# Kernel optimization log

Hardware: AMD Instinct MI355X
Metric: run time of the kernel (lower is better)

The kernel has to match this reference:

```python
import jax, jax.numpy as jnp
import numpy as np

NUM_HEADS = 8
POOL = 4  # kq_downscale kernel/stride (spatial)
B, S, H, W, C = 32, 8, 32, 32, 128
TOTAL_KEY_DEPTH = 512
VAL_FILTERS = 128
OUT_FILTERS = 64


def _avg_pool(x):
    # tf.nn.avg_pool3d with kernel/stride [1,1,4,4,1], SAME padding (dims divide evenly)
    win = (1, 1, POOL, POOL, 1)
    s = jax.lax.reduce_window(x, 0.0, jax.lax.add, win, win, 'SAME')
    return s / (POOL * POOL)


def _conv2d(x, w, b):
    # TimeDistributed Conv2D, same padding. x: (B,S,H,W,Cin), w: (kh,kw,Cin,Cout)
    Bx, Sx, Hx, Wx, Cx = x.shape
    y = jax.lax.conv_general_dilated(
        x.reshape(Bx * Sx, Hx, Wx, Cx), w, (1, 1), 'SAME',
        dimension_numbers=('NHWC', 'HWIO', 'NHWC'))
    return y.reshape(Bx, Sx, Hx, Wx, -1) + b


def _rel_emb(length_q, length_k, max_rel, table):
    # _generate_relative_positions_embeddings
    rk = jnp.arange(length_k)
    rq = rk[-length_q:]
    idx = jnp.clip(rk[None, :] - rq[:, None], -max_rel, max_rel) + max_rel
    return table[idx]  # (Lq, Lk, depth)


def setup_inputs() -> dict:
    key = jax.random.key(0)
    ks = jax.random.split(key, 11)
    qk_in = (H // POOL) * (W // POOL) * C          # 8*8*128 = 8192
    d_vh = H * W * VAL_FILTERS // NUM_HEADS         # 16384 per-head value depth
    d_kh = TOTAL_KEY_DEPTH // NUM_HEADS             # 64
    return {
        'inputs': jax.random.normal(ks[0], (B, 1, H, W, C), jnp.float32),
        'k_antecedent': jax.random.normal(ks[1], (B, S, H, W, C), jnp.float32),
        'v_antecedent': jax.random.normal(ks[2], (B, S, H, W, C), jnp.float32),
        'w_q': jax.random.normal(ks[3], (qk_in, TOTAL_KEY_DEPTH), jnp.float32) * 0.02,
        'w_k': jax.random.normal(ks[4], (qk_in, TOTAL_KEY_DEPTH), jnp.float32) * 0.02,
        'conv_v_w': jax.random.normal(ks[5], (3, 3, C, VAL_FILTERS), jnp.float32) * 0.02,
        'conv_v_b': jnp.zeros((VAL_FILTERS,), jnp.float32),
        'conv_o_w': jax.random.normal(ks[6], (3, 3, VAL_FILTERS, OUT_FILTERS), jnp.float32) * 0.02,
        'conv_o_b': jnp.zeros((OUT_FILTERS,), jnp.float32),
        'table_k': jax.random.normal(ks[7], (S, d_kh), jnp.float32) * 0.05,
        'table_v': jax.random.normal(ks[8], (S, d_vh), jnp.float32) * 0.05,
    }


def reference(inputs, k_antecedent, v_antecedent, w_q, w_k,
              conv_v_w, conv_v_b, conv_o_w, conv_o_b, table_k, table_v):
    Bx, Sx, Hx, Wx, Cx = v_antecedent.shape
    nh = NUM_HEADS
    max_rel = Sx // 2 - 1  # attn_factor_reduc/2 - 1

    # downscale + flatten q/k antecedents
    q_a = _avg_pool(inputs).reshape(Bx, 1, -1)
    k_a = _avg_pool(k_antecedent).reshape(Bx, Sx, -1)
    q = q_a @ w_q                   # (B,1,Dk)
    k = k_a @ w_k                   # (B,S,Dk)
    v = _conv2d(v_antecedent, conv_v_w, conv_v_b).reshape(Bx, Sx, -1)  # (B,S,Dv)

    def split(x):  # (B,L,D) -> (B,h,L,D/h)
        Bz, L, D = x.shape
        return x.reshape(Bz, L, nh, D // nh).transpose(0, 2, 1, 3)

    q, k, v = split(q), split(k), split(v)
    q = q * (q.shape[-1] ** -0.5)

    # relative-position logits: _relative_attention_inner(q, k, z_k, transpose=True)
    z_k = _rel_emb(1, Sx, max_rel, table_k)  # (1,S,dkh)
    logits = jnp.einsum('bhqd,bhkd->bhqk', q, k) + jnp.einsum('bhqd,qkd->bhqk', q, z_k)
    weights = jax.nn.softmax(logits, axis=-1)  # (B,h,1,S)

    # relative values: _relative_attention_inner(weights, v, z_v, transpose=False)
    z_v = _rel_emb(1, Sx, max_rel, table_v)  # (1,S,dvh)
    x = jnp.einsum('bhqk,bhkd->bhqd', weights, v) + jnp.einsum('bhqk,qkd->bhqd', weights, z_v)

    # combine heads, restore spatial shape, output conv
    x = x.transpose(0, 2, 1, 3).reshape(Bx, 1, Hx, Wx, -1)  # (B,1,H,W,Fv)
    out = _conv2d(x, conv_o_w, conv_o_b)                     # (B,1,H,W,Fo)
    return out
```

## Files before the change

### kernel.cpp

```cpp
#include <hip/hip_runtime.h>
#include <hip/hip_bf16.h>

typedef __hip_bfloat16 bf16;
typedef __attribute__((ext_vector_type(8))) short bf16x8;
typedef __attribute__((ext_vector_type(4))) float f32x4;

constexpr int B_ = 32, S_ = 8, H_ = 32, W_ = 32, C_ = 128;
constexpr int NH_ = 8, KD_ = 512, DKH_ = 64, VF_ = 128, OF_ = 64;
constexpr int QKIN_ = 8192;

static __device__ __forceinline__ short bfbits(float f) {
    bf16 h = __float2bfloat16(f);
    short s;
    __builtin_memcpy(&s, &h, 2);
    return s;
}
static __device__ __forceinline__ unsigned int packbf2(float a, float b) {
    return ((unsigned int)(unsigned short)bfbits(b) << 16) | (unsigned short)bfbits(a);
}

__global__ void k_zero(float* __restrict__ p, int n) {
    int i = blockIdx.x * 256 + threadIdx.x;
    if (i < n) p[i] = 0.f;
}

__global__ void k_pool4(const float* __restrict__ in, short* __restrict__ out, int n_img) {
    int idx = blockIdx.x * 256 + threadIdx.x;
    if (idx >= n_img * 2048) return;
    int c4 = (idx & 31) * 4;
    int pw = (idx >> 5) & 7;
    int ph = (idx >> 8) & 7;
    int img = idx >> 11;
    const float* p = in + (((size_t)img * H_ + ph * 4) * W_ + pw * 4) * C_ + c4;
    float4 s = {0.f, 0.f, 0.f, 0.f};
#pragma unroll
    for (int dy = 0; dy < 4; ++dy)
#pragma unroll
        for (int dx = 0; dx < 4; ++dx) {
            float4 v = *reinterpret_cast<const float4*>(p + (dy * W_ + dx) * C_);
            s.x += v.x; s.y += v.y; s.z += v.z; s.w += v.w;
        }
    uint2 pk;
    pk.x = packbf2(s.x * 0.0625f, s.y * 0.0625f);
    pk.y = packbf2(s.z * 0.0625f, s.w * 0.0625f);
    *reinterpret_cast<uint2*>(out + (size_t)img * QKIN_ + (ph * 8 + pw) * 128 + c4) = pk;
}

__global__ __launch_bounds__(256) void k_wT(const float* __restrict__ w,
                                            short* __restrict__ wT) {
    __shared__ float t[64][65];
    int k0 = blockIdx.x * 64, n0 = blockIdx.y * 64;
    int col = threadIdx.x & 63, r4 = threadIdx.x >> 6;
#pragma unroll
    for (int i = 0; i < 16; ++i) {
        int kr = i * 4 + r4;
        t[kr][col] = w[(size_t)(k0 + kr) * KD_ + n0 + col];
    }
    __syncthreads();
    int n = threadIdx.x >> 3, kg = threadIdx.x & 7;
#pragma unroll
    for (int half = 0; half < 2; ++half) {
        int nn = n + half * 32;
        short v[8];
#pragma unroll
        for (int j = 0; j < 8; ++j) v[j] = bfbits(t[kg * 8 + j][nn]);
        *reinterpret_cast<bf16x8*>(wT + (size_t)(n0 + nn) * QKIN_ + k0 + kg * 8) =
            *reinterpret_cast<bf16x8*>(v);
    }
}

__global__ __launch_bounds__(256) void k_gemm_mfma(const short* __restrict__ A,
                                                   const short* __restrict__ WT,
                                                   float* __restrict__ out) {
    int wave = threadIdx.x >> 6, lane = threadIdx.x & 63;
    int quad = lane >> 4, l15 = lane & 15;
    int m0 = blockIdx.x * 32;
    int n0 = blockIdx.y * 128 + wave * 32;
    int k0 = blockIdx.z * 1024;
    f32x4 acc[2][2];
#pragma unroll
    for (int mt = 0; mt < 2; ++mt)
#pragma unroll
        for (int nt = 0; nt < 2; ++nt) acc[mt][nt] = (f32x4){0.f, 0.f, 0.f, 0.f};
    const short* a0p = A + (size_t)(m0 + l15) * QKIN_;
    const short* a1p = a0p + 16 * QKIN_;
    const short* b0p = WT + (size_t)(n0 + l15) * QKIN_;
    const short* b1p = b0p + 16 * QKIN_;
    for (int kk = k0 + quad * 8; kk < k0 + 1024; kk += 32) {
        bf16x8 a0 = *reinterpret_cast<const bf16x8*>(a0p + kk);
        bf16x8 a1 = *reinterpret_cast<const bf16x8*>(a1p + kk);
        bf16x8 b0 = *reinterpret_cast<const bf16x8*>(b0p + kk);
        bf16x8 b1 = *reinterpret_cast<const bf16x8*>(b1p + kk);
        acc[0][0] = __builtin_amdgcn_mfma_f32_16x16x32_bf16(a0, b0, acc[0][0], 0, 0, 0);
        acc[0][1] = __builtin_amdgcn_mfma_f32_16x16x32_bf16(a0, b1, acc[0][1], 0, 0, 0);
        acc[1][0] = __builtin_amdgcn_mfma_f32_16x16x32_bf16(a1, b0, acc[1][0], 0, 0, 0);
        acc[1][1] = __builtin_amdgcn_mfma_f32_16x16x32_bf16(a1, b1, acc[1][1], 0, 0, 0);
    }
#pragma unroll
    for (int mt = 0; mt < 2; ++mt)
#pragma unroll
        for (int nt = 0; nt < 2; ++nt)
#pragma unroll
            for (int reg = 0; reg < 4; ++reg)
                atomicAdd(&out[(size_t)(m0 + mt * 16 + quad * 4 + reg) * KD_ +
                               n0 + nt * 16 + l15],
                          acc[mt][nt][reg]);
}

__global__ void k_attnw(const float* __restrict__ q, const float* __restrict__ k,
                        const float* __restrict__ table_k, float* __restrict__ wt) {
    int b = blockIdx.x;
    int t = threadIdx.x;
    int h = t >> 3, s = t & 7;
    int zi = (s < 4) ? 0 : (s - 4);
    const float* qp = q + (size_t)b * KD_ + h * DKH_;
    const float* kp = k + ((size_t)b * S_ + s) * KD_ + h * DKH_;
    const float* zp = table_k + (size_t)zi * DKH_;
    float dot = 0.f;
    for (int d = 0; d < DKH_; ++d)
        dot += qp[d] * (kp[d] + zp[d]);
    dot *= 0.125f;
    float m = dot;
    for (int msk = 1; msk < 8; msk <<= 1) m = fmaxf(m, __shfl_xor(m, msk));
    float e = expf(dot - m);
    float sum = e;
    for (int msk = 1; msk < 8; msk <<= 1) sum += __shfl_xor(sum, msk);
    wt[((size_t)b * NH_ + h) * S_ + s] = e / sum;
}

template <int CO>
__global__ void k_wtrans(const float* __restrict__ in, short* __restrict__ out) {
    int idx = blockIdx.x * 256 + threadIdx.x;
    if (idx >= 9 * 128 * CO) return;
    int tap = idx / (128 * CO);
    int rem = idx % (128 * CO);
    int co = rem / 128;
    int ci = rem % 128;
    out[idx] = bfbits(in[((size_t)tap * 128 + ci) * CO + co]);
}

__global__ __launch_bounds__(256) void k_convv_mfma(
    const float* __restrict__ v_ant, const short* __restrict__ wvT,
    const float* __restrict__ bias, const float* __restrict__ tbv,
    const float* __restrict__ wt, short* __restrict__ x) {
    __shared__ short strip[6 * 32 * 136];
    int b = blockIdx.x >> 3, h = blockIdx.x & 7;
    int y0 = 4 * h;
    const float* wtb = wt + (size_t)(b * NH_ + h) * S_;
    float w8[8];
#pragma unroll
    for (int kk = 0; kk < 8; ++kk) w8[kk] = wtb[kk];
    for (int i = threadIdx.x; i < 6 * 1024; i += 256) {
        int r = i >> 10, rem = i & 1023;
        int yimg = y0 - 1 + r;
        float4 s = {0.f, 0.f, 0.f, 0.f};
        if (0 <= yimg && yimg < H_) {
            const float* base = v_ant + (size_t)b * 1048576 + yimg * 4096 + rem * 4;
#pragma unroll
            for (int kk = 0; kk < 8; ++kk) {
                float4 v = *reinterpret_cast<const float4*>(base + (size_t)kk * 131072);
                s.x = fmaf(w8[kk], v.x, s.x);
                s.y = fmaf(w8[kk], v.y, s.y);
                s.z = fmaf(w8[kk], v.z, s.z);
                s.w = fmaf(w8[kk], v.w, s.w);
            }
        }
        int px = rem >> 5, cg = rem & 31;
        uint2 pk;
        pk.x = packbf2(s.x, s.y);
        pk.y = packbf2(s.z, s.w);
        *reinterpret_cast<uint2*>(&strip[(r * 32 + px) * 136 + cg * 4]) = pk;
    }
    __syncthreads();
    int wave = threadIdx.x >> 6, lane = threadIdx.x & 63;
    int quad = lane >> 4, l15 = lane & 15;
    int n0 = wave * 32;
    f32x4 acc[8][2];
#pragma unroll
    for (int mt = 0; mt < 8; ++mt)
#pragma unroll
        for (int nt = 0; nt < 2; ++nt) acc[mt][nt] = (f32x4){0.f, 0.f, 0.f, 0.f};
    const bf16x8 zero8 = (bf16x8)0;
    for (int kc = 0; kc < 36; ++kc) {
        int tap = kc >> 2;
        int ci0 = (kc & 3) * 32 + quad * 8;
        int ky = tap / 3, dx = tap % 3;
        bf16x8 bfr[2];
#pragma unroll
        for (int nt = 0; nt < 2; ++nt) {
            int co = n0 + nt * 16 + l15;
            bfr[nt] = *reinterpret_cast<const bf16x8*>(
                wvT + ((size_t)tap * 128 + co) * 128 + ci0);
        }
#pragma unroll
        for (int mt = 0; mt < 8; ++mt) {
            int jout = mt >> 1, half = mt & 1;
            int r = jout + ky;
            int pxg = half * 16 + l15 + dx - 1;
            bf16x8 afr = zero8;
            if (pxg >= 0 && pxg < 32)
                afr = *reinterpret_cast<const bf16x8*>(
                    &strip[(r * 32 + pxg) * 136 + ci0]);
            acc[mt][0] = __builtin_amdgcn_mfma_f32_16x16x32_bf16(afr, bfr[0], acc[mt][0], 0, 0, 0);
            acc[mt][1] = __builtin_amdgcn_mfma_f32_16x16x32_bf16(afr, bfr[1], acc[mt][1], 0, 0, 0);
        }
    }
    float cw[4];
    cw[0] = w8[0] + w8[1] + w8[2] + w8[3] + w8[4];
    cw[1] = w8[5];
    cw[2] = w8[6];
    cw[3] = w8[7];
#pragma unroll
    for (int mt = 0; mt < 8; ++mt) {
        int jout = mt >> 1, half = mt & 1;
#pragma unroll
        for (int nt = 0; nt < 2; ++nt) {
            int co = n0 + nt * 16 + l15;
            float bv = bias[co];
#pragma unroll
            for (int reg = 0; reg < 4; ++reg) {
                int px = half * 16 + quad * 4 + reg;
                int d = jout * 4096 + px * 128 + co;
                float v = acc[mt][nt][reg] + bv;
                v = fmaf(cw[0], tbv[d], v);
                v = fmaf(cw[1], tbv[16384 + d], v);
                v = fmaf(cw[2], tbv[32768 + d], v);
                v = fmaf(cw[3], tbv[49152 + d], v);
                x[(((size_t)b * H_ + y0 + jout) * W_ + px) * C_ + co] = bfbits(v);
            }
        }
    }
}

__global__ __launch_bounds__(256) void k_convo_mfma(
    const short* __restrict__ x, const short* __restrict__ woT,
    const float* __restrict__ bias, float* __restrict__ out) {
    __shared__ short strip[6 * 32 * 136];
    int b = blockIdx.x >> 3, rg = blockIdx.x & 7;
    int y0 = 4 * rg;
    for (int i = threadIdx.x; i < 6 * 1024; i += 256) {
        int r = i >> 10, rem = i & 1023;
        int yimg = y0 - 1 + r;
        uint2 v = {0u, 0u};
        if (0 <= yimg && yimg < H_)
            v = *reinterpret_cast<const uint2*>(
                x + (size_t)b * 131072 + yimg * 4096 + rem * 4);
        int px = rem >> 5, cg = rem & 31;
        *reinterpret_cast<uint2*>(&strip[(r * 32 + px) * 136 + cg * 4]) = v;
    }
    __syncthreads();
    int wave = threadIdx.x >> 6, lane = threadIdx.x & 63;
    int quad = lane >> 4, l15 = lane & 15;
    int co = wave * 16 + l15;
    f32x4 acc[8];
#pragma unroll
    for (int mt = 0; mt < 8; ++mt) acc[mt] = (f32x4){0.f, 0.f, 0.f, 0.f};
    const bf16x8 zero8 = (bf16x8)0;
    for (int kc = 0; kc < 36; ++kc) {
        int tap = kc >> 2;
        int ci0 = (kc & 3) * 32 + quad * 8;
        int ky = tap / 3, dx = tap % 3;
        bf16x8 bfr = *reinterpret_cast<const bf16x8*>(
            woT + ((size_t)tap * 64 + co) * 128 + ci0);
#pragma unroll
        for (int mt = 0; mt < 8; ++mt) {
            int jout = mt >> 1, half = mt & 1;
            int r = jout + ky;
            int pxg = half * 16 + l15 + dx - 1;
            bf16x8 afr = zero8;
            if (pxg >= 0 && pxg < 32)
                afr = *reinterpret_cast<const bf16x8*>(
                    &strip[(r * 32 + pxg) * 136 + ci0]);
            acc[mt] = __builtin_amdgcn_mfma_f32_16x16x32_bf16(afr, bfr, acc[mt], 0, 0, 0);
        }
    }
    float bv = bias[co];
#pragma unroll
    for (int mt = 0; mt < 8; ++mt) {
        int jout = mt >> 1, half = mt & 1;
#pragma unroll
        for (int reg = 0; reg < 4; ++reg) {
            int px = half * 16 + quad * 4 + reg;
            out[(((size_t)b * H_ + y0 + jout) * W_ + px) * OF_ + co] = acc[mt][reg] + bv;
        }
    }
}

extern "C" void kernel_launch(void* const* d_in, const int* in_sizes, int n_in,
                              void* d_out, int out_size, void* d_ws, size_t ws_size,
                              hipStream_t stream) {
    const float* inp   = (const float*)d_in[0];
    const float* k_ant = (const float*)d_in[1];
    const float* v_ant = (const float*)d_in[2];
    const float* w_q   = (const float*)d_in[3];
    const float* w_k   = (const float*)d_in[4];
    const float* cvw   = (const float*)d_in[5];
    const float* cvb   = (const float*)d_in[6];
    const float* cow   = (const float*)d_in[7];
    const float* cob   = (const float*)d_in[8];
    const float* tbk   = (const float*)d_in[9];
    const float* tbv   = (const float*)d_in[10];

    char* wsb = (char*)d_ws;
    float* q    = (float*)(wsb + 0);
    float* k    = (float*)(wsb + 65536);
    float* wt   = (float*)(wsb + 589824);
    short* q_a  = (short*)(wsb + 598016);
    short* k_a  = (short*)(wsb + 1122304);
    short* wvT  = (short*)(wsb + 5316608);
    short* woT  = (short*)(wsb + 5611520);
    short* wkT  = (short*)(wsb + 5758976);
    short* wqT  = (short*)(wsb + 14147584);
    short* x    = wqT;

    k_zero<<<576, 256, 0, stream>>>(q, 147456);
    k_pool4<<<256, 256, 0, stream>>>(inp, q_a, 32);
    k_pool4<<<2048, 256, 0, stream>>>(k_ant, k_a, 256);
    k_wT<<<dim3(128, 8), 256, 0, stream>>>(w_q, wqT);
    k_wT<<<dim3(128, 8), 256, 0, stream>>>(w_k, wkT);
    k_wtrans<128><<<576, 256, 0, stream>>>(cvw, wvT);
    k_wtrans<64><<<288, 256, 0, stream>>>(cow, woT);
    k_gemm_mfma<<<dim3(1, 4, 8), 256, 0, stream>>>(q_a, wqT, q);
    k_gemm_mfma<<<dim3(8, 4, 8), 256, 0, stream>>>(k_a, wkT, k);
    k_attnw<<<32, 64, 0, stream>>>(q, k, tbk, wt);
    k_convv_mfma<<<256, 256, 0, stream>>>(v_ant, wvT, cvb, tbv, wt, x);
    k_convo_mfma<<<256, 256, 0, stream>>>(x, woT, cob, (float*)d_out);
}
```

Measured before the change: 434.9 us.

## Merge prep kernels, fuse Q/K GEMMs, fold softmax into value conv, pad strips

The seven preprocessing launches (zeroing, pooling, weight transposes) become one block-dispatched prep kernel. The Q and K projection GEMMs merge into a single launch with a finer K split (512), which gives more blocks and more atomics. The attention-weight softmax is computed inside the value conv kernel by one wave per block, so the separate kernel and its buffer go away. Both conv kernels add zero-padded halo columns in shared memory to remove the bounds checks in the MFMA inner loop, at the cost of slightly more LDS.

```diff
diff --git a/kernel.cpp b/kernel.cpp
--- a/kernel.cpp
+++ b/kernel.cpp
@@ -19,14 +19,9 @@
     return ((unsigned int)(unsigned short)bfbits(b) << 16) | (unsigned short)bfbits(a);
 }
 
-__global__ void k_zero(float* __restrict__ p, int n) {
-    int i = blockIdx.x * 256 + threadIdx.x;
-    if (i < n) p[i] = 0.f;
-}
-
-__global__ void k_pool4(const float* __restrict__ in, short* __restrict__ out, int n_img) {
-    int idx = blockIdx.x * 256 + threadIdx.x;
-    if (idx >= n_img * 2048) return;
+
+static __device__ __forceinline__ void dev_pool4(const float* __restrict__ in,
+                                                 short* __restrict__ out, int idx) {
     int c4 = (idx & 31) * 4;
     int pw = (idx >> 5) & 7;
     int ph = (idx >> 8) & 7;
@@ -46,10 +41,10 @@
     *reinterpret_cast<uint2*>(out + (size_t)img * QKIN_ + (ph * 8 + pw) * 128 + c4) = pk;
 }
 
-__global__ __launch_bounds__(256) void k_wT(const float* __restrict__ w,
-                                            short* __restrict__ wT) {
-    __shared__ float t[64][65];
-    int k0 = blockIdx.x * 64, n0 = blockIdx.y * 64;
+static __device__ __forceinline__ void dev_wT(const float* __restrict__ w,
+                                              short* __restrict__ wT, int local,
+                                              float (*t)[65]) {
+    int k0 = (local >> 3) * 64, n0 = (local & 7) * 64;
     int col = threadIdx.x & 63, r4 = threadIdx.x >> 6;
 #pragma unroll
     for (int i = 0; i < 16; ++i) {
@@ -69,14 +64,73 @@
     }
 }
 
-__global__ __launch_bounds__(256) void k_gemm_mfma(const short* __restrict__ A,
-                                                   const short* __restrict__ WT,
-                                                   float* __restrict__ out) {
+static __device__ __forceinline__ void dev_wtrans(const float* __restrict__ in,
+                                                  short* __restrict__ out, int idx,
+                                                  int CO) {
+    int tap = idx / (128 * CO);
+    int rem = idx % (128 * CO);
+    int co = rem / 128;
+    int ci = rem & 127;
+    out[idx] = bfbits(in[((size_t)tap * 128 + ci) * CO + co]);
+}
+
+constexpr int PB_ZERO  = 144;
+constexpr int PB_POOLI = PB_ZERO + 256;
+constexpr int PB_POOLK = PB_POOLI + 2048;
+constexpr int PB_WTQ   = PB_POOLK + 1024;
+constexpr int PB_WTK   = PB_WTQ + 1024;
+constexpr int PB_WV    = PB_WTK + 576;
+constexpr int PB_WO    = PB_WV + 288;
+
+__global__ __launch_bounds__(256) void k_prep(
+    const float* __restrict__ inp, const float* __restrict__ k_ant,
+    const float* __restrict__ w_q, const float* __restrict__ w_k,
+    const float* __restrict__ cvw, const float* __restrict__ cow,
+    float* __restrict__ qk_zero, short* __restrict__ q_a, short* __restrict__ k_a,
+    short* __restrict__ wqT, short* __restrict__ wkT,
+    short* __restrict__ wvT, short* __restrict__ woT) {
+    __shared__ float t[64][65];
+    int bx = blockIdx.x;
+    if (bx < PB_ZERO) {
+        int i = (bx * 256 + threadIdx.x) * 4;
+        float4 z = {0.f, 0.f, 0.f, 0.f};
+        *reinterpret_cast<float4*>(qk_zero + i) = z;
+    } else if (bx < PB_POOLI) {
+        dev_pool4(inp, q_a, (bx - PB_ZERO) * 256 + threadIdx.x);
+    } else if (bx < PB_POOLK) {
+        dev_pool4(k_ant, k_a, (bx - PB_POOLI) * 256 + threadIdx.x);
+    } else if (bx < PB_WTK) {
+        if (bx < PB_WTQ)
+            dev_wT(w_q, wqT, bx - PB_POOLK, t);
+        else
+            dev_wT(w_k, wkT, bx - PB_WTQ, t);
+    } else if (bx < PB_WV) {
+        dev_wtrans(cvw, wvT, (bx - PB_WTK) * 256 + threadIdx.x, 128);
+    } else {
+        dev_wtrans(cow, woT, (bx - PB_WV) * 256 + threadIdx.x, 64);
+    }
+}
+
+__global__ __launch_bounds__(256) void k_gemm2(
+    const short* __restrict__ qa, const short* __restrict__ ka,
+    const short* __restrict__ wqTp, const short* __restrict__ wkTp,
+    float* __restrict__ qo, float* __restrict__ ko) {
     int wave = threadIdx.x >> 6, lane = threadIdx.x & 63;
     int quad = lane >> 4, l15 = lane & 15;
-    int m0 = blockIdx.x * 32;
-    int n0 = blockIdx.y * 128 + wave * 32;
-    int k0 = blockIdx.z * 1024;
+    int id = blockIdx.x;
+    const short* A;
+    const short* WT;
+    float* out;
+    int m0, rem;
+    if (id < 64) {
+        A = qa; WT = wqTp; out = qo; m0 = 0; rem = id;
+    } else {
+        id -= 64;
+        A = ka; WT = wkTp; out = ko;
+        m0 = (id >> 6) * 32; rem = id & 63;
+    }
+    int n0 = (rem & 3) * 128 + wave * 32;
+    int k0 = (rem >> 2) * 512;
     f32x4 acc[2][2];
 #pragma unroll
     for (int mt = 0; mt < 2; ++mt)
@@ -86,7 +140,7 @@
     const short* a1p = a0p + 16 * QKIN_;
     const short* b0p = WT + (size_t)(n0 + l15) * QKIN_;
     const short* b1p = b0p + 16 * QKIN_;
-    for (int kk = k0 + quad * 8; kk < k0 + 1024; kk += 32) {
+    for (int kk = k0 + quad * 8; kk < k0 + 512; kk += 32) {
         bf16x8 a0 = *reinterpret_cast<const bf16x8*>(a0p + kk);
         bf16x8 a1 = *reinterpret_cast<const bf16x8*>(a1p + kk);
         bf16x8 b0 = *reinterpret_cast<const bf16x8*>(b0p + kk);
@@ -107,49 +161,52 @@
                           acc[mt][nt][reg]);
 }
 
-__global__ void k_attnw(const float* __restrict__ q, const float* __restrict__ k,
-                        const float* __restrict__ table_k, float* __restrict__ wt) {
-    int b = blockIdx.x;
-    int t = threadIdx.x;
-    int h = t >> 3, s = t & 7;
-    int zi = (s < 4) ? 0 : (s - 4);
-    const float* qp = q + (size_t)b * KD_ + h * DKH_;
-    const float* kp = k + ((size_t)b * S_ + s) * KD_ + h * DKH_;
-    const float* zp = table_k + (size_t)zi * DKH_;
-    float dot = 0.f;
-    for (int d = 0; d < DKH_; ++d)
-        dot += qp[d] * (kp[d] + zp[d]);
-    dot *= 0.125f;
-    float m = dot;
-    for (int msk = 1; msk < 8; msk <<= 1) m = fmaxf(m, __shfl_xor(m, msk));
-    float e = expf(dot - m);
-    float sum = e;
-    for (int msk = 1; msk < 8; msk <<= 1) sum += __shfl_xor(sum, msk);
-    wt[((size_t)b * NH_ + h) * S_ + s] = e / sum;
-}
-
-template <int CO>
-__global__ void k_wtrans(const float* __restrict__ in, short* __restrict__ out) {
-    int idx = blockIdx.x * 256 + threadIdx.x;
-    if (idx >= 9 * 128 * CO) return;
-    int tap = idx / (128 * CO);
-    int rem = idx % (128 * CO);
-    int co = rem / 128;
-    int ci = rem % 128;
-    out[idx] = bfbits(in[((size_t)tap * 128 + ci) * CO + co]);
-}
-
 __global__ __launch_bounds__(256) void k_convv_mfma(
     const float* __restrict__ v_ant, const short* __restrict__ wvT,
     const float* __restrict__ bias, const float* __restrict__ tbv,
-    const float* __restrict__ wt, short* __restrict__ x) {
-    __shared__ short strip[6 * 32 * 136];
+    const float* __restrict__ q, const float* __restrict__ kmat,
+    const float* __restrict__ tbk, short* __restrict__ x) {
+    __shared__ short strip[6 * 34 * 136];
+    __shared__ float w8s[8];
     int b = blockIdx.x >> 3, h = blockIdx.x & 7;
     int y0 = 4 * h;
-    const float* wtb = wt + (size_t)(b * NH_ + h) * S_;
+    if (threadIdx.x < 64) {
+        int d = threadIdx.x;
+        float qv = q[(size_t)b * KD_ + h * DKH_ + d];
+        float lg[8];
+        float m = -1e30f;
+#pragma unroll
+        for (int s = 0; s < 8; ++s) {
+            int zi = (s < 4) ? 0 : (s - 4);
+            float kv = kmat[((size_t)b * S_ + s) * KD_ + h * DKH_ + d] + tbk[zi * DKH_ + d];
+            float p = qv * kv * 0.125f;
+#pragma unroll
+            for (int msk = 1; msk < 64; msk <<= 1) p += __shfl_xor(p, msk);
+            lg[s] = p;
+            m = fmaxf(m, p);
+        }
+        float sum = 0.f;
+#pragma unroll
+        for (int s = 0; s < 8; ++s) {
+            lg[s] = expf(lg[s] - m);
+            sum += lg[s];
+        }
+        if (d == 0) {
+            float inv = 1.f / sum;
+#pragma unroll
+            for (int s = 0; s < 8; ++s) w8s[s] = lg[s] * inv;
+        }
+    }
+    for (int i = threadIdx.x; i < 384; i += 256) {
+        int r = i >> 6, remz = i & 63;
+        int side = remz >> 5, cg = remz & 31;
+        uint2 z = {0u, 0u};
+        *reinterpret_cast<uint2*>(&strip[(r * 34 + side * 33) * 136 + cg * 4]) = z;
+    }
+    __syncthreads();
     float w8[8];
 #pragma unroll
-    for (int kk = 0; kk < 8; ++kk) w8[kk] = wtb[kk];
+    for (int kk = 0; kk < 8; ++kk) w8[kk] = w8s[kk];
     for (int i = threadIdx.x; i < 6 * 1024; i += 256) {
         int r = i >> 10, rem = i & 1023;
         int yimg = y0 - 1 + r;
@@ -169,7 +226,7 @@
         uint2 pk;
         pk.x = packbf2(s.x, s.y);
         pk.y = packbf2(s.z, s.w);
-        *reinterpret_cast<uint2*>(&strip[(r * 32 + px) * 136 + cg * 4]) = pk;
+        *reinterpret_cast<uint2*>(&strip[(r * 34 + px + 1) * 136 + cg * 4]) = pk;
     }
     __syncthreads();
     int wave = threadIdx.x >> 6, lane = threadIdx.x & 63;
@@ -180,7 +237,6 @@
     for (int mt = 0; mt < 8; ++mt)
 #pragma unroll
         for (int nt = 0; nt < 2; ++nt) acc[mt][nt] = (f32x4){0.f, 0.f, 0.f, 0.f};
-    const bf16x8 zero8 = (bf16x8)0;
     for (int kc = 0; kc < 36; ++kc) {
         int tap = kc >> 2;
         int ci0 = (kc & 3) * 32 + quad * 8;
@@ -196,11 +252,9 @@
         for (int mt = 0; mt < 8; ++mt) {
             int jout = mt >> 1, half = mt & 1;
             int r = jout + ky;
-            int pxg = half * 16 + l15 + dx - 1;
-            bf16x8 afr = zero8;
-            if (pxg >= 0 && pxg < 32)
-                afr = *reinterpret_cast<const bf16x8*>(
-                    &strip[(r * 32 + pxg) * 136 + ci0]);
+            int px1 = half * 16 + l15 + dx;
+            bf16x8 afr = *reinterpret_cast<const bf16x8*>(
+                &strip[(r * 34 + px1) * 136 + ci0]);
             acc[mt][0] = __builtin_amdgcn_mfma_f32_16x16x32_bf16(afr, bfr[0], acc[mt][0], 0, 0, 0);
             acc[mt][1] = __builtin_amdgcn_mfma_f32_16x16x32_bf16(afr, bfr[1], acc[mt][1], 0, 0, 0);
         }
@@ -235,9 +289,15 @@
 __global__ __launch_bounds__(256) void k_convo_mfma(
     const short* __restrict__ x, const short* __restrict__ woT,
     const float* __restrict__ bias, float* __restrict__ out) {
-    __shared__ short strip[6 * 32 * 136];
+    __shared__ short strip[6 * 34 * 136];
     int b = blockIdx.x >> 3, rg = blockIdx.x & 7;
     int y0 = 4 * rg;
+    for (int i = threadIdx.x; i < 384; i += 256) {
+        int r = i >> 6, remz = i & 63;
+        int side = remz >> 5, cg = remz & 31;
+        uint2 z = {0u, 0u};
+        *reinterpret_cast<uint2*>(&strip[(r * 34 + side * 33) * 136 + cg * 4]) = z;
+    }
     for (int i = threadIdx.x; i < 6 * 1024; i += 256) {
         int r = i >> 10, rem = i & 1023;
         int yimg = y0 - 1 + r;
@@ -246,7 +306,7 @@
             v = *reinterpret_cast<const uint2*>(
                 x + (size_t)b * 131072 + yimg * 4096 + rem * 4);
         int px = rem >> 5, cg = rem & 31;
-        *reinterpret_cast<uint2*>(&strip[(r * 32 + px) * 136 + cg * 4]) = v;
+        *reinterpret_cast<uint2*>(&strip[(r * 34 + px + 1) * 136 + cg * 4]) = v;
     }
     __syncthreads();
     int wave = threadIdx.x >> 6, lane = threadIdx.x & 63;
@@ -255,7 +315,6 @@
     f32x4 acc[8];
 #pragma unroll
     for (int mt = 0; mt < 8; ++mt) acc[mt] = (f32x4){0.f, 0.f, 0.f, 0.f};
-    const bf16x8 zero8 = (bf16x8)0;
     for (int kc = 0; kc < 36; ++kc) {
         int tap = kc >> 2;
         int ci0 = (kc & 3) * 32 + quad * 8;
@@ -266,11 +325,9 @@
         for (int mt = 0; mt < 8; ++mt) {
             int jout = mt >> 1, half = mt & 1;
             int r = jout + ky;
-            int pxg = half * 16 + l15 + dx - 1;
-            bf16x8 afr = zero8;
-            if (pxg >= 0 && pxg < 32)
-                afr = *reinterpret_cast<const bf16x8*>(
-                    &strip[(r * 32 + pxg) * 136 + ci0]);
+            int px1 = half * 16 + l15 + dx;
+            bf16x8 afr = *reinterpret_cast<const bf16x8*>(
+                &strip[(r * 34 + px1) * 136 + ci0]);
             acc[mt] = __builtin_amdgcn_mfma_f32_16x16x32_bf16(afr, bfr, acc[mt], 0, 0, 0);
         }
     }
@@ -304,7 +361,6 @@
     char* wsb = (char*)d_ws;
     float* q    = (float*)(wsb + 0);
     float* k    = (float*)(wsb + 65536);
-    float* wt   = (float*)(wsb + 589824);
     short* q_a  = (short*)(wsb + 598016);
     short* k_a  = (short*)(wsb + 1122304);
     short* wvT  = (short*)(wsb + 5316608);
@@ -313,16 +369,9 @@
     short* wqT  = (short*)(wsb + 14147584);
     short* x    = wqT;
 
-    k_zero<<<576, 256, 0, stream>>>(q, 147456);
-    k_pool4<<<256, 256, 0, stream>>>(inp, q_a, 32);
-    k_pool4<<<2048, 256, 0, stream>>>(k_ant, k_a, 256);
-    k_wT<<<dim3(128, 8), 256, 0, stream>>>(w_q, wqT);
-    k_wT<<<dim3(128, 8), 256, 0, stream>>>(w_k, wkT);
-    k_wtrans<128><<<576, 256, 0, stream>>>(cvw, wvT);
-    k_wtrans<64><<<288, 256, 0, stream>>>(cow, woT);
-    k_gemm_mfma<<<dim3(1, 4, 8), 256, 0, stream>>>(q_a, wqT, q);
-    k_gemm_mfma<<<dim3(8, 4, 8), 256, 0, stream>>>(k_a, wkT, k);
-    k_attnw<<<32, 64, 0, stream>>>(q, k, tbk, wt);
-    k_convv_mfma<<<256, 256, 0, stream>>>(v_ant, wvT, cvb, tbv, wt, x);
+    k_prep<<<PB_WO, 256, 0, stream>>>(inp, k_ant, w_q, w_k, cvw, cow,
+                                      q, q_a, k_a, wqT, wkT, wvT, woT);
+    k_gemm2<<<576, 256, 0, stream>>>(q_a, k_a, wqT, wkT, q, k);
+    k_convv_mfma<<<256, 256, 0, stream>>>(v_ant, wvT, cvb, tbv, q, k, tbk, x);
     k_convo_mfma<<<256, 256, 0, stream>>>(x, woT, cob, (float*)d_out);
 }
```

New measurement: 400.6 us. -7.9%, faster.
